# Optimization experiments

Hardware: AMD Instinct MI355X
Metric: run time of the kernel (lower is better)

## Reference

```python
import jax, jax.numpy as jnp
import numpy as np

D = 256        # d_model
NH = 8         # nhead
L = 2          # num_layers
FF = 1024      # dim_feedforward
HD = D // NH   # head dim
LN_EPS = 1e-5
M_EPS = 1e-9


def setup_inputs() -> dict:
    key = jax.random.key(0)
    ks = jax.random.split(key, 8)
    B, N, E = 8, 1024, 16384
    s = 0.02
    inp = {
        "H": jax.random.normal(ks[0], (B, N, D), jnp.float32),
        "edge_index": jax.random.randint(ks[1], (B, 2, E), 0, N),
        "m": jax.random.uniform(ks[2], (B, E), jnp.float32),
        # transformer encoder params, stacked over layers
        "Wqkv": jax.random.normal(ks[3], (L, 3 * D, D), jnp.float32) * s,
        "bqkv": jnp.zeros((L, 3 * D), jnp.float32),
        "Wo": jax.random.normal(ks[4], (L, D, D), jnp.float32) * s,
        "bo": jnp.zeros((L, D), jnp.float32),
        "ln1_w": jnp.ones((L, D), jnp.float32),
        "ln1_b": jnp.zeros((L, D), jnp.float32),
        "W1": jax.random.normal(ks[5], (L, FF, D), jnp.float32) * s,
        "b1": jnp.zeros((L, FF), jnp.float32),
        "W2": jax.random.normal(ks[6], (L, D, FF), jnp.float32) * s,
        "b2": jnp.zeros((L, D), jnp.float32),
        "ln2_w": jnp.ones((L, D), jnp.float32),
        "ln2_b": jnp.zeros((L, D), jnp.float32),
        "lnf_w": jnp.ones((D,), jnp.float32),
        "lnf_b": jnp.zeros((D,), jnp.float32),
    }
    return inp


def layer_norm(x, w, b):
    mu = jnp.mean(x, axis=-1, keepdims=True)
    var = jnp.mean(jnp.square(x - mu), axis=-1, keepdims=True)
    return (x - mu) * jax.lax.rsqrt(var + LN_EPS) * w + b


def build_bias(edge_index, m, N):
    # per-graph: -inf everywhere, 0 on diag, log(m+eps) symmetrically on edges
    bias = jnp.full((N, N), -jnp.inf, jnp.float32)
    d = jnp.arange(N)
    bias = bias.at[d, d].set(0.0)
    bv = jnp.log(m + M_EPS)
    row, col = edge_index[0], edge_index[1]
    bias = bias.at[row, col].set(bv)
    bias = bias.at[col, row].set(bv)
    return bias


def mha(x, bias, Wqkv, bqkv, Wo, bo):
    B, N, d = x.shape
    qkv = x @ Wqkv.T + bqkv                          # [B,N,3D]
    q, k, v = jnp.split(qkv, 3, axis=-1)
    def heads(t):
        return t.reshape(B, N, NH, HD).transpose(0, 2, 1, 3)  # [B,NH,N,HD]
    q, k, v = heads(q), heads(k), heads(v)
    scores = jnp.einsum("bhnd,bhmd->bhnm", q, k) / np.sqrt(HD)
    scores = scores + bias[:, None]                  # same bias for all heads
    attn = jax.nn.softmax(scores, axis=-1)
    out = jnp.einsum("bhnm,bhmd->bhnd", attn, v)
    out = out.transpose(0, 2, 1, 3).reshape(B, N, d)
    return out @ Wo.T + bo


def reference(H, edge_index, m, Wqkv, bqkv, Wo, bo, ln1_w, ln1_b, W1, b1,
              W2, b2, ln2_w, ln2_b, lnf_w, lnf_b):
    B, N, _ = H.shape
    bias = jax.vmap(lambda ei, mm: build_bias(ei, mm, N))(edge_index, m)  # [B,N,N]
    x = H
    for l in range(L):  # small fixed layer count
        a = mha(x, bias, Wqkv[l], bqkv[l], Wo[l], bo[l])
        x = layer_norm(x + a, ln1_w[l], ln1_b[l])
        f = jax.nn.gelu(x @ W1[l].T + b1[l], approximate=False) @ W2[l].T + b2[l]
        x = layer_norm(x + f, ln2_w[l], ln2_b[l])
    return layer_norm(x, lnf_w, lnf_b)
```

## Files before the change

kernel.cpp:

```cpp
#include <hip/hip_runtime.h>
#include <hip/hip_bf16.h>
#include <math.h>

typedef __bf16 bf16_t;
typedef __attribute__((ext_vector_type(8))) __bf16 bf16x8;
typedef __attribute__((ext_vector_type(4))) __bf16 bf16x4;
typedef __attribute__((ext_vector_type(4))) float f32x4;

#define BATCH 8
#define NTOK 1024
#define NEDGE 16384
#define CAP 96

__device__ __forceinline__ void gload_lds16(const void* g, void* l) {
  __builtin_amdgcn_global_load_lds(
      (const __attribute__((address_space(1))) unsigned int*)(uintptr_t)g,
      (__attribute__((address_space(3))) unsigned int*)(unsigned int)(uintptr_t)l,
      16, 0, 0);
}

__global__ void k_pre(int4* __restrict__ cnt,
                      const float* __restrict__ H, const float* __restrict__ Wqkv,
                      const float* __restrict__ Wo, const float* __restrict__ W1,
                      const float* __restrict__ W2, bf16_t* __restrict__ xb,
                      bf16_t* __restrict__ wqkvb, bf16_t* __restrict__ wob,
                      bf16_t* __restrict__ w1b, bf16_t* __restrict__ w2b) {
  int i = blockIdx.x * 256 + threadIdx.x;
  if (blockIdx.x < 8) {
    int4 z = {0, 0, 0, 0};
    cnt[i] = z;
  }
  const float* s; bf16_t* d; int off;
  if (i < 524288)      { s = H;    d = xb;    off = i; }
  else if (i < 622592) { s = Wqkv; d = wqkvb; off = i - 524288; }
  else if (i < 655360) { s = Wo;   d = wob;   off = i - 622592; }
  else if (i < 786432) { s = W1;   d = w1b;   off = i - 655360; }
  else if (i < 917504) { s = W2;   d = w2b;   off = i - 786432; }
  else return;
  float4 v = ((const float4*)s)[off];
  bf16x4 o;
  o[0] = (bf16_t)v.x; o[1] = (bf16_t)v.y; o[2] = (bf16_t)v.z; o[3] = (bf16_t)v.w;
  ((bf16x4*)d)[off] = o;
}

__global__ void k_scatter2(const int* __restrict__ ei, int* __restrict__ cnt,
                           int* __restrict__ ent) {
  int idx = blockIdx.x * 256 + threadIdx.x;
  if (idx >= BATCH * NEDGE) return;
  int b = idx >> 14;
  int e = idx & (NEDGE - 1);
  const int* eb = ei + (size_t)b * 2 * NEDGE;
  int r = eb[e], c = eb[NEDGE + e];
  int rowr = (b << 10) + r, rowc = (b << 10) + c;
  int q = atomicAdd(cnt + rowr, 1);
  if (q < CAP) ent[rowr * CAP + q] = ((e + 1) << 10) | c;
  q = atomicAdd(cnt + rowc, 1);
  if (q < CAP) ent[rowc * CAP + q] = ((NEDGE + e + 1) << 10) | r;
}

__global__ __launch_bounds__(256) void k_build2(
    const int* __restrict__ cnt, const int* __restrict__ ent,
    const float* __restrict__ mptr,
    int* __restrict__ nbcol, float* __restrict__ nbval, int* __restrict__ nbcnt) {
  const int w = threadIdx.x >> 6;
  const int l = threadIdx.x & 63;
  const int row = blockIdx.x * 4 + w;
  const int i = row & 1023;
  const int b = row >> 10;
  __shared__ int sE[4][CAP];
  __shared__ int sW[4][CAP];
  const int n = min(cnt[row], CAP);
  for (int j = l; j < n; j += 64) sE[w][j] = ent[(size_t)row * CAP + j];
  __syncthreads();

  bool dcov_l = false;
  bool win[2] = {false, false};
  int myc[2], myp[2];
#pragma unroll
  for (int s = 0; s < 2; ++s) {
    int k = s * 64 + l;
    if (k < n) {
      int pk = sE[w][k], ck = pk & 1023;
      myc[s] = ck; myp[s] = pk;
      bool wn = true;
      for (int j = 0; j < n; ++j) {
        int pj = sE[w][j];
        if ((pj & 1023) == ck && pj > pk) wn = false;
      }
      win[s] = wn;
      sW[w][k] = wn ? 1 : 0;
      if (ck == i) dcov_l = true;
    }
  }
  const bool dcov = __any(dcov_l);
  unsigned long long m0 = __ballot(win[0]);
  unsigned long long m1 = __ballot(win[1]);
  if (l == 0) nbcnt[row] = __popcll(m0) + __popcll(m1) + (dcov ? 0 : 1);

#pragma unroll
  for (int s = 0; s < 2; ++s) {
    int k = s * 64 + l;
    if (k < n && win[s]) {
      int pos = 0;
      for (int j = 0; j < n; ++j)
        if (sW[w][j] && (sE[w][j] & 1023) < myc[s]) ++pos;
      if (!dcov && i < myc[s]) ++pos;
      int e = ((myp[s] >> 10) - 1) & (NEDGE - 1);
      float v = logf(mptr[(size_t)b * NEDGE + e] + 1e-9f);
      if (pos < CAP) {
        nbcol[(size_t)row * CAP + pos] = myc[s];
        nbval[(size_t)row * CAP + pos] = v;
      }
    }
  }
  if (!dcov && l == 0) {
    int pos = 0;
    for (int j = 0; j < n; ++j)
      if (sW[w][j] && (sE[w][j] & 1023) < i) ++pos;
    nbcol[(size_t)row * CAP + pos] = i;
    nbval[(size_t)row * CAP + pos] = 0.f;
  }
}

template <int EPI, int BM>
__global__ __launch_bounds__(256) void gemm_bt(
    const bf16_t* __restrict__ A, const bf16_t* __restrict__ Bw,
    const float* __restrict__ bias, bf16_t* __restrict__ Cb,
    int M, int N, int K) {
  constexpr int MI = BM / 32;
  __shared__ bf16_t As[2][BM * 64];
  __shared__ bf16_t Bs[2][128 * 64];
  const int t = threadIdx.x;
  const int l = t & 63;
  const int w = t >> 6;
  const int wr = w >> 1, wc = w & 1;
  const int bm = blockIdx.y * BM, bn = blockIdx.x * 128;

  f32x4 acc[MI][4] = {};

  auto stage = [&](int buf, int k0) {
#pragma unroll
    for (int i = 0; i < BM / 32; ++i) {
      int idx = i * 2048 + t * 8;
      int row = idx >> 6, col = idx & 63;
      gload_lds16(A + (size_t)(bm + row) * K + (k0 + col), (void*)(&As[buf][0] + i * 2048 + w * 512));
    }
#pragma unroll
    for (int i = 0; i < 4; ++i) {
      int idx = i * 2048 + t * 8;
      int row = idx >> 6, col = idx & 63;
      gload_lds16(Bw + (size_t)(bn + row) * K + (k0 + col), (void*)(&Bs[buf][0] + i * 2048 + w * 512));
    }
  };

  const int nt = K >> 6;
  stage(0, 0);
  asm volatile("s_waitcnt vmcnt(0)" ::: "memory");
  __syncthreads();
  for (int kt = 0; kt < nt; ++kt) {
    const int cur = kt & 1;
    if (kt + 1 < nt) stage(cur ^ 1, (kt + 1) << 6);
#pragma unroll
    for (int kk = 0; kk < 2; ++kk) {
      bf16x8 af[MI], bfr[4];
#pragma unroll
      for (int mi = 0; mi < MI; ++mi)
        af[mi] = *(const bf16x8*)(&As[cur][0] + (wr * (BM / 2) + mi * 16 + (l & 15)) * 64 + kk * 32 + (l >> 4) * 8);
#pragma unroll
      for (int ni = 0; ni < 4; ++ni)
        bfr[ni] = *(const bf16x8*)(&Bs[cur][0] + (wc * 64 + ni * 16 + (l & 15)) * 64 + kk * 32 + (l >> 4) * 8);
#pragma unroll
      for (int mi = 0; mi < MI; ++mi)
#pragma unroll
        for (int ni = 0; ni < 4; ++ni)
          acc[mi][ni] = __builtin_amdgcn_mfma_f32_16x16x32_bf16(af[mi], bfr[ni], acc[mi][ni], 0, 0, 0);
    }
    asm volatile("s_waitcnt vmcnt(0)" ::: "memory");
    __syncthreads();
  }

  const int r0 = (l >> 4) * 4;
  const int cc = l & 15;
#pragma unroll
  for (int mi = 0; mi < MI; ++mi) {
#pragma unroll
    for (int ni = 0; ni < 4; ++ni) {
      int col = bn + wc * 64 + ni * 16 + cc;
      float bv = bias[col];
#pragma unroll
      for (int r = 0; r < 4; ++r) {
        int row = bm + wr * (BM / 2) + mi * 16 + r0 + r;
        float v = acc[mi][ni][r] + bv;
        if (EPI == 1)
          v = 0.5f * v * (1.f + erff(v * 0.70710678118654752f));
        Cb[(size_t)row * N + col] = (bf16_t)v;
      }
    }
  }
}

__global__ __launch_bounds__(256) void k_attn_oproj(
    const bf16_t* __restrict__ qkvb,
    const int* __restrict__ nbcol, const float* __restrict__ nbval,
    const int* __restrict__ nbcnt,
    const bf16_t* __restrict__ Wo, const float* __restrict__ bo,
    const bf16_t* __restrict__ residb,
    const float* __restrict__ lnw, const float* __restrict__ lnb,
    bf16_t* __restrict__ xbout) {
  __shared__ __align__(16) char smem[57856];
  bf16_t* Bs    = (bf16_t*)smem;
  bf16_t* ao    = (bf16_t*)(smem + 32768);
  float*  s_s   = (float*)(smem + 41216);
  int*    s_col = (int*)(smem + 53632);
  float*  s_bia = (float*)(smem + 55168);
  float*  E     = (float*)(smem + 41216);
  const int t = threadIdx.x, l = t & 63, w = t >> 6;
  const int b = blockIdx.x & 7;
  const int bm = (b << 10) + (blockIdx.x >> 3) * 16;

  auto stageB = [&](int k0) {
#pragma unroll
    for (int i = 0; i < 8; ++i) {
      int rr = (w * 8 + i) * 8 + (l >> 3), col = (l & 7) * 8;
      gload_lds16(Wo + (size_t)rr * 256 + (k0 + col), (void*)(Bs + (w * 8 + i) * 512));
    }
  };
  stageB(0);

  const float scale = 0.17677669529663687f;
  const int h1 = l & 7;
  for (int rr = 0; rr < 4; ++rr) {
    const int row = bm + w * 4 + rr;
    const int deg = nbcnt[row];
    asm volatile("s_waitcnt lgkmcnt(0)" ::: "memory");
    for (int j = l; j < deg; j += 64) {
      s_col[w * 96 + j] = nbcol[(size_t)row * CAP + j];
      s_bia[w * 96 + j] = nbval[(size_t)row * CAP + j];
    }
    float q[32];
    {
      const bf16x8* qp = (const bf16x8*)(qkvb + (size_t)row * 768 + h1 * 32);
#pragma unroll
      for (int u = 0; u < 4; ++u) {
        bf16x8 t8 = qp[u];
#pragma unroll
        for (int j = 0; j < 8; ++j) q[u * 8 + j] = (float)t8[j];
      }
    }
    asm volatile("s_waitcnt lgkmcnt(0)" ::: "memory");

    const int nit = (deg + 7) >> 3;
    float mx = -INFINITY;
    for (int it = 0; it < nit; ++it) {
      int idx = it * 8 + (l >> 3);
      float sc = -INFINITY;
      if (idx < deg) {
        int col = s_col[w * 96 + idx];
        const bf16x8* kr = (const bf16x8*)(qkvb + ((size_t)((b << 10) + col)) * 768 + 256 + h1 * 32);
        float d = 0.f;
#pragma unroll
        for (int u = 0; u < 4; ++u) {
          bf16x8 kv = kr[u];
#pragma unroll
          for (int j = 0; j < 8; ++j) d += (float)kv[j] * q[u * 8 + j];
        }
        sc = d * scale + s_bia[w * 96 + idx];
        s_s[(w * 8 + h1) * 97 + idx] = sc;
      }
      mx = fmaxf(mx, sc);
    }
#pragma unroll
    for (int o = 8; o < 64; o <<= 1) mx = fmaxf(mx, __shfl_xor(mx, o));
    asm volatile("s_waitcnt lgkmcnt(0)" ::: "memory");
    float lsum = 0.f;
    for (int it = 0; it < nit; ++it) {
      int idx = it * 8 + (l >> 3);
      if (idx < deg) {
        float p = __expf(s_s[(w * 8 + h1) * 97 + idx] - mx);
        s_s[(w * 8 + h1) * 97 + idx] = p;
        lsum += p;
      }
    }
#pragma unroll
    for (int o = 8; o < 64; o <<= 1) lsum += __shfl_xor(lsum, o);
    const int h3 = l >> 3;
    float den = __shfl(lsum, h3);
    asm volatile("s_waitcnt lgkmcnt(0)" ::: "memory");
    float a0 = 0.f, a1 = 0.f, a2 = 0.f, a3 = 0.f;
    const bf16_t* vbase = qkvb + ((size_t)(b << 10)) * 768 + 512 + l * 4;
#pragma unroll 4
    for (int idx = 0; idx < deg; ++idx) {
      float p = s_s[(w * 8 + h3) * 97 + idx];
      bf16x4 vv = *(const bf16x4*)(vbase + (size_t)s_col[w * 96 + idx] * 768);
      a0 += p * (float)vv[0]; a1 += p * (float)vv[1];
      a2 += p * (float)vv[2]; a3 += p * (float)vv[3];
    }
    float rden = 1.f / den;
    bf16x4 o4;
    o4[0] = (bf16_t)(a0 * rden); o4[1] = (bf16_t)(a1 * rden);
    o4[2] = (bf16_t)(a2 * rden); o4[3] = (bf16_t)(a3 * rden);
    *(bf16x4*)(ao + (w * 4 + rr) * 264 + l * 4) = o4;
  }
  asm volatile("s_waitcnt vmcnt(0) lgkmcnt(0)" ::: "memory");
  __syncthreads();

  f32x4 acc[4] = {};
  for (int kt = 0; kt < 4; ++kt) {
#pragma unroll
    for (int kk = 0; kk < 2; ++kk) {
      bf16x8 af = *(const bf16x8*)(ao + (l & 15) * 264 + kt * 64 + kk * 32 + (l >> 4) * 8);
#pragma unroll
      for (int ni = 0; ni < 4; ++ni) {
        bf16x8 bfr = *(const bf16x8*)(Bs + (w * 64 + ni * 16 + (l & 15)) * 64 + kk * 32 + (l >> 4) * 8);
        acc[ni] = __builtin_amdgcn_mfma_f32_16x16x32_bf16(af, bfr, acc[ni], 0, 0, 0);
      }
    }
    __syncthreads();
    if (kt < 3) {
      stageB((kt + 1) * 64);
      asm volatile("s_waitcnt vmcnt(0)" ::: "memory");
      __syncthreads();
    }
  }

  const int r0 = (l >> 4) * 4;
  const int cc = l & 15;
#pragma unroll
  for (int ni = 0; ni < 4; ++ni) {
    int col = w * 64 + ni * 16 + cc;
    float bv = bo[col];
#pragma unroll
    for (int r = 0; r < 4; ++r)
      E[(r0 + r) * 258 + col] = acc[ni][r] + bv;
  }
  __syncthreads();

  const int row = t >> 4;
  const int sub = t & 15;
  const float* ep = E + row * 258 + sub * 16;
  const bf16_t* rp = residb + (size_t)(bm + row) * 256 + sub * 16;
  float v[16];
  float s = 0.f;
#pragma unroll
  for (int j = 0; j < 4; ++j) {
    float4 a4 = ((const float4*)ep)[j];
    bf16x4 r4 = ((const bf16x4*)rp)[j];
    v[j * 4 + 0] = a4.x + (float)r4[0]; v[j * 4 + 1] = a4.y + (float)r4[1];
    v[j * 4 + 2] = a4.z + (float)r4[2]; v[j * 4 + 3] = a4.w + (float)r4[3];
    s += v[j * 4 + 0] + v[j * 4 + 1] + v[j * 4 + 2] + v[j * 4 + 3];
  }
#pragma unroll
  for (int o = 1; o < 16; o <<= 1) s += __shfl_xor(s, o);
  float mu = s * (1.f / 256.f);
  float e2 = 0.f;
#pragma unroll
  for (int j = 0; j < 16; ++j) { float d = v[j] - mu; e2 += d * d; }
#pragma unroll
  for (int o = 1; o < 16; o <<= 1) e2 += __shfl_xor(e2, o);
  float rs = rsqrtf(e2 * (1.f / 256.f) + 1e-5f);
  bf16_t* xbo = xbout + (size_t)(bm + row) * 256 + sub * 16;
#pragma unroll
  for (int j = 0; j < 4; ++j) {
    float4 w4 = ((const float4*)(lnw + sub * 16))[j];
    float4 b4 = ((const float4*)(lnb + sub * 16))[j];
    bf16x4 ob;
    ob[0] = (bf16_t)((v[j * 4 + 0] - mu) * rs * w4.x + b4.x);
    ob[1] = (bf16_t)((v[j * 4 + 1] - mu) * rs * w4.y + b4.y);
    ob[2] = (bf16_t)((v[j * 4 + 2] - mu) * rs * w4.z + b4.z);
    ob[3] = (bf16_t)((v[j * 4 + 3] - mu) * rs * w4.w + b4.w);
    ((bf16x4*)xbo)[j] = ob;
  }
}

template <int FIN>
__global__ __launch_bounds__(256) void gemm_ln(
    const bf16_t* __restrict__ A, const bf16_t* __restrict__ Bw,
    const float* __restrict__ bias, const bf16_t* __restrict__ residb,
    const float* __restrict__ lnw, const float* __restrict__ lnb,
    const float* __restrict__ lnfw, const float* __restrict__ lnfb,
    bf16_t* __restrict__ xbout, float* __restrict__ outf, int K) {
  __shared__ __align__(16) char smem[69632];
  bf16_t* As = (bf16_t*)smem;
  bf16_t* Bs = (bf16_t*)(smem + 4096);
  float*  E  = (float*)smem;
  const int t = threadIdx.x;
  const int l = t & 63;
  const int w = t >> 6;
  const int bm = blockIdx.x * 16;

  f32x4 acc[4] = {};

  auto stage = [&](int buf, int k0) {
    if (w < 2) {
      int row = w * 8 + (l >> 3), col = (l & 7) * 8;
      gload_lds16(A + (size_t)(bm + row) * K + (k0 + col), (void*)(As + buf * 1024 + w * 512));
    }
#pragma unroll
    for (int i = 0; i < 8; ++i) {
      int rr = (w * 8 + i) * 8 + (l >> 3), col = (l & 7) * 8;
      gload_lds16(Bw + (size_t)rr * K + (k0 + col), (void*)(Bs + buf * 16384 + (w * 8 + i) * 512));
    }
  };

  const int nt = K >> 6;
  stage(0, 0);
  asm volatile("s_waitcnt vmcnt(0)" ::: "memory");
  __syncthreads();
  for (int kt = 0; kt < nt; ++kt) {
    const int cur = kt & 1;
    if (kt + 1 < nt) stage(cur ^ 1, (kt + 1) << 6);
#pragma unroll
    for (int kk = 0; kk < 2; ++kk) {
      bf16x8 af = *(const bf16x8*)(As + cur * 1024 + (l & 15) * 64 + kk * 32 + (l >> 4) * 8);
#pragma unroll
      for (int ni = 0; ni < 4; ++ni) {
        bf16x8 bfr = *(const bf16x8*)(Bs + cur * 16384 + (w * 64 + ni * 16 + (l & 15)) * 64 + kk * 32 + (l >> 4) * 8);
        acc[ni] = __builtin_amdgcn_mfma_f32_16x16x32_bf16(af, bfr, acc[ni], 0, 0, 0);
      }
    }
    asm volatile("s_waitcnt vmcnt(0)" ::: "memory");
    __syncthreads();
  }

  const int r0 = (l >> 4) * 4;
  const int cc = l & 15;
#pragma unroll
  for (int ni = 0; ni < 4; ++ni) {
    int col = w * 64 + ni * 16 + cc;
    float bv = bias[col];
#pragma unroll
    for (int r = 0; r < 4; ++r)
      E[(r0 + r) * 258 + col] = acc[ni][r] + bv;
  }
  __syncthreads();

  const int row = t >> 4;
  const int sub = t & 15;
  const float* ep = E + row * 258 + sub * 16;
  const bf16_t* rp = residb + (size_t)(bm + row) * 256 + sub * 16;
  float v[16];
  float s = 0.f;
#pragma unroll
  for (int j = 0; j < 4; ++j) {
    float4 a4 = ((const float4*)ep)[j];
    bf16x4 r4 = ((const bf16x4*)rp)[j];
    v[j * 4 + 0] = a4.x + (float)r4[0]; v[j * 4 + 1] = a4.y + (float)r4[1];
    v[j * 4 + 2] = a4.z + (float)r4[2]; v[j * 4 + 3] = a4.w + (float)r4[3];
    s += v[j * 4 + 0] + v[j * 4 + 1] + v[j * 4 + 2] + v[j * 4 + 3];
  }
#pragma unroll
  for (int o = 1; o < 16; o <<= 1) s += __shfl_xor(s, o);
  float mu = s * (1.f / 256.f);
  float e2 = 0.f;
#pragma unroll
  for (int j = 0; j < 16; ++j) { float d = v[j] - mu; e2 += d * d; }
#pragma unroll
  for (int o = 1; o < 16; o <<= 1) e2 += __shfl_xor(e2, o);
  float rs = rsqrtf(e2 * (1.f / 256.f) + 1e-5f);
  float y[16];
#pragma unroll
  for (int j = 0; j < 4; ++j) {
    float4 w4 = ((const float4*)(lnw + sub * 16))[j];
    float4 b4 = ((const float4*)(lnb + sub * 16))[j];
    y[j * 4 + 0] = (v[j * 4 + 0] - mu) * rs * w4.x + b4.x;
    y[j * 4 + 1] = (v[j * 4 + 1] - mu) * rs * w4.y + b4.y;
    y[j * 4 + 2] = (v[j * 4 + 2] - mu) * rs * w4.z + b4.z;
    y[j * 4 + 3] = (v[j * 4 + 3] - mu) * rs * w4.w + b4.w;
  }
  if (FIN == 0) {
    bf16_t* xbo = xbout + (size_t)(bm + row) * 256 + sub * 16;
#pragma unroll
    for (int j = 0; j < 4; ++j) {
      bf16x4 ob;
      ob[0] = (bf16_t)y[j * 4 + 0]; ob[1] = (bf16_t)y[j * 4 + 1];
      ob[2] = (bf16_t)y[j * 4 + 2]; ob[3] = (bf16_t)y[j * 4 + 3];
      ((bf16x4*)xbo)[j] = ob;
    }
  } else {
    float s2 = 0.f;
#pragma unroll
    for (int j = 0; j < 16; ++j) s2 += y[j];
#pragma unroll
    for (int o = 1; o < 16; o <<= 1) s2 += __shfl_xor(s2, o);
    float mu2 = s2 * (1.f / 256.f);
    float q2 = 0.f;
#pragma unroll
    for (int j = 0; j < 16; ++j) { float d = y[j] - mu2; q2 += d * d; }
#pragma unroll
    for (int o = 1; o < 16; o <<= 1) q2 += __shfl_xor(q2, o);
    float rs2 = rsqrtf(q2 * (1.f / 256.f) + 1e-5f);
    float* xo = outf + (size_t)(bm + row) * 256 + sub * 16;
#pragma unroll
    for (int j = 0; j < 4; ++j) {
      float4 w4 = ((const float4*)(lnfw + sub * 16))[j];
      float4 b4 = ((const float4*)(lnfb + sub * 16))[j];
      float4 o4 = {(y[j * 4 + 0] - mu2) * rs2 * w4.x + b4.x,
                   (y[j * 4 + 1] - mu2) * rs2 * w4.y + b4.y,
                   (y[j * 4 + 2] - mu2) * rs2 * w4.z + b4.z,
                   (y[j * 4 + 3] - mu2) * rs2 * w4.w + b4.w};
      ((float4*)xo)[j] = o4;
    }
  }
}

extern "C" void kernel_launch(void* const* d_in, const int* in_sizes, int n_in,
                              void* d_out, int out_size, void* d_ws, size_t ws_size,
                              hipStream_t stream) {
  const float* H    = (const float*)d_in[0];
  const int*   ei   = (const int*)d_in[1];
  const float* m    = (const float*)d_in[2];
  const float* Wqkv = (const float*)d_in[3];
  const float* bqkv = (const float*)d_in[4];
  const float* Wo   = (const float*)d_in[5];
  const float* bo   = (const float*)d_in[6];
  const float* ln1w = (const float*)d_in[7];
  const float* ln1b = (const float*)d_in[8];
  const float* W1   = (const float*)d_in[9];
  const float* b1   = (const float*)d_in[10];
  const float* W2   = (const float*)d_in[11];
  const float* b2   = (const float*)d_in[12];
  const float* ln2w = (const float*)d_in[13];
  const float* ln2b = (const float*)d_in[14];
  const float* lnfw = (const float*)d_in[15];
  const float* lnfb = (const float*)d_in[16];

  char* ws = (char*)d_ws;
  size_t off = 0;
  auto alloc = [&](size_t bytes) {
    void* p = ws + off;
    off += (bytes + 255) & ~(size_t)255;
    return p;
  };

  int*    cnt   = (int*)alloc((size_t)BATCH * NTOK * 4);
  int*    ent   = (int*)alloc((size_t)BATCH * NTOK * CAP * 4);
  int*    nbcol = (int*)alloc((size_t)BATCH * NTOK * CAP * 4);
  float*  nbval = (float*)alloc((size_t)BATCH * NTOK * CAP * 4);
  int*    nbcnt = (int*)alloc((size_t)BATCH * NTOK * 4);
  bf16_t* qkvb  = (bf16_t*)alloc((size_t)8192 * 768 * 2);
  bf16_t* wqkvb = (bf16_t*)alloc((size_t)2 * 768 * 256 * 2);
  bf16_t* wob   = (bf16_t*)alloc((size_t)2 * 256 * 256 * 2);
  bf16_t* w1b   = (bf16_t*)alloc((size_t)2 * 1024 * 256 * 2);
  bf16_t* w2b   = (bf16_t*)alloc((size_t)2 * 256 * 1024 * 2);
  bf16_t* xb    = (bf16_t*)alloc((size_t)8192 * 256 * 2);
  bf16_t* x1b   = (bf16_t*)alloc((size_t)8192 * 256 * 2);
  bf16_t* ffb   = (bf16_t*)alloc((size_t)8192 * 1024 * 2);

  k_pre<<<3584, 256, 0, stream>>>((int4*)cnt, H, Wqkv, Wo, W1, W2,
                                  xb, wqkvb, wob, w1b, w2b);
  k_scatter2<<<(BATCH * NEDGE + 255) / 256, 256, 0, stream>>>(ei, cnt, ent);
  k_build2<<<BATCH * NTOK / 4, 256, 0, stream>>>(cnt, ent, m, nbcol, nbval, nbcnt);

  for (int lyr = 0; lyr < 2; ++lyr) {
    gemm_bt<3, 64><<<dim3(768 / 128, 8192 / 64), 256, 0, stream>>>(
        xb, wqkvb + (size_t)lyr * 768 * 256, bqkv + lyr * 768, qkvb, 8192, 768, 256);
    k_attn_oproj<<<512, 256, 0, stream>>>(
        qkvb, nbcol, nbval, nbcnt,
        wob + (size_t)lyr * 256 * 256, bo + lyr * 256, xb,
        ln1w + lyr * 256, ln1b + lyr * 256, x1b);
    gemm_bt<1, 128><<<dim3(1024 / 128, 8192 / 128), 256, 0, stream>>>(
        x1b, w1b + (size_t)lyr * 1024 * 256, b1 + lyr * 1024, ffb, 8192, 1024, 256);
    if (lyr == 0) {
      gemm_ln<0><<<512, 256, 0, stream>>>(
          ffb, w2b + (size_t)lyr * 256 * 1024, b2 + lyr * 256, x1b,
          ln2w + lyr * 256, ln2b + lyr * 256, nullptr, nullptr, xb, nullptr, 1024);
    } else {
      gemm_ln<1><<<512, 256, 0, stream>>>(
          ffb, w2b + (size_t)lyr * 256 * 1024, b2 + lyr * 256, x1b,
          ln2w + lyr * 256, ln2b + lyr * 256, lnfw, lnfb, nullptr, (float*)d_out, 1024);
    }
  }
}
```

Before: 195.1 us.

## Stream W2 fragments into registers and preload full A tile in gemm_ln

The FFN down-projection+LayerNorm kernel no longer stages B (weight) tiles through shared memory with per-iteration barriers. Each wave now loads its weight fragments straight from global memory into a triple-buffered register ring. The full 16x1024 A row-block is loaded into padded LDS once up front. This removes most barriers and cuts LDS footprint, which should raise occupancy. The cost is higher register pressure and uncoalesced-ish direct global loads of weights, which are re-read by all 512 blocks and depend on L2 hits.

After: 232.0 us. +18.9%, slower.

```diff
diff --git a/kernel.cpp b/kernel.cpp
--- a/kernel.cpp
+++ b/kernel.cpp
@@ -378,49 +378,52 @@
     const float* __restrict__ bias, const bf16_t* __restrict__ residb,
     const float* __restrict__ lnw, const float* __restrict__ lnb,
     const float* __restrict__ lnfw, const float* __restrict__ lnfb,
-    bf16_t* __restrict__ xbout, float* __restrict__ outf, int K) {
-  __shared__ __align__(16) char smem[69632];
+    bf16_t* __restrict__ xbout, float* __restrict__ outf) {
+  constexpr int K = 1024, NT = 16;
+  __shared__ __align__(16) char smem[33024];
   bf16_t* As = (bf16_t*)smem;
-  bf16_t* Bs = (bf16_t*)(smem + 4096);
   float*  E  = (float*)smem;
   const int t = threadIdx.x;
   const int l = t & 63;
   const int w = t >> 6;
   const int bm = blockIdx.x * 16;
 
+#pragma unroll
+  for (int c = 0; c < 8; ++c) {
+    int f = t + c * 256;
+    int row = f >> 7, c16 = f & 127;
+    bf16x8 v = *(const bf16x8*)(A + (size_t)(bm + row) * K + c16 * 8);
+    *(bf16x8*)(As + row * 1032 + c16 * 8) = v;
+  }
+  __syncthreads();
+
   f32x4 acc[4] = {};
-
-  auto stage = [&](int buf, int k0) {
-    if (w < 2) {
-      int row = w * 8 + (l >> 3), col = (l & 7) * 8;
-      gload_lds16(A + (size_t)(bm + row) * K + (k0 + col), (void*)(As + buf * 1024 + w * 512));
-    }
-#pragma unroll
-    for (int i = 0; i < 8; ++i) {
-      int rr = (w * 8 + i) * 8 + (l >> 3), col = (l & 7) * 8;
-      gload_lds16(Bw + (size_t)rr * K + (k0 + col), (void*)(Bs + buf * 16384 + (w * 8 + i) * 512));
-    }
-  };
-
-  const int nt = K >> 6;
-  stage(0, 0);
-  asm volatile("s_waitcnt vmcnt(0)" ::: "memory");
-  __syncthreads();
-  for (int kt = 0; kt < nt; ++kt) {
-    const int cur = kt & 1;
-    if (kt + 1 < nt) stage(cur ^ 1, (kt + 1) << 6);
+  bf16x8 breg[3][8];
+  const bf16_t* bbase = Bw + (size_t)(w * 64 + (l & 15)) * K + (l >> 4) * 8;
+#define LOADB(slot, kt)                                                        \
+  {                                                                            \
+    _Pragma("unroll")                                                          \
+    for (int ni = 0; ni < 4; ++ni)                                             \
+      _Pragma("unroll")                                                        \
+      for (int kk = 0; kk < 2; ++kk)                                           \
+        breg[slot][ni * 2 + kk] =                                              \
+            *(const bf16x8*)(bbase + (size_t)(ni * 16) * K + (kt) * 64 + kk * 32); \
+  }
+  LOADB(0, 0)
+  LOADB(1, 1)
+#pragma unroll
+  for (int kt = 0; kt < NT; ++kt) {
+    if (kt + 2 < NT) LOADB((kt + 2) % 3, kt + 2)
 #pragma unroll
     for (int kk = 0; kk < 2; ++kk) {
-      bf16x8 af = *(const bf16x8*)(As + cur * 1024 + (l & 15) * 64 + kk * 32 + (l >> 4) * 8);
-#pragma unroll
-      for (int ni = 0; ni < 4; ++ni) {
-        bf16x8 bfr = *(const bf16x8*)(Bs + cur * 16384 + (w * 64 + ni * 16 + (l & 15)) * 64 + kk * 32 + (l >> 4) * 8);
-        acc[ni] = __builtin_amdgcn_mfma_f32_16x16x32_bf16(af, bfr, acc[ni], 0, 0, 0);
-      }
-    }
-    asm volatile("s_waitcnt vmcnt(0)" ::: "memory");
-    __syncthreads();
-  }
+      bf16x8 af = *(const bf16x8*)(As + (l & 15) * 1032 + kt * 64 + kk * 32 + (l >> 4) * 8);
+#pragma unroll
+      for (int ni = 0; ni < 4; ++ni)
+        acc[ni] = __builtin_amdgcn_mfma_f32_16x16x32_bf16(af, breg[kt % 3][ni * 2 + kk], acc[ni], 0, 0, 0);
+    }
+  }
+#undef LOADB
+  __syncthreads();
 
   const int r0 = (l >> 4) * 4;
   const int cc = l & 15;
@@ -563,11 +566,11 @@
     if (lyr == 0) {
       gemm_ln<0><<<512, 256, 0, stream>>>(
           ffb, w2b + (size_t)lyr * 256 * 1024, b2 + lyr * 256, x1b,
-          ln2w + lyr * 256, ln2b + lyr * 256, nullptr, nullptr, xb, nullptr, 1024);
+          ln2w + lyr * 256, ln2b + lyr * 256, nullptr, nullptr, xb, nullptr);
     } else {
       gemm_ln<1><<<512, 256, 0, stream>>>(
           ffb, w2b + (size_t)lyr * 256 * 1024, b2 + lyr * 256, x1b,
-          ln2w + lyr * 256, ln2b + lyr * 256, lnfw, lnfb, nullptr, (float*)d_out, 1024);
-    }
-  }
-}
+          ln2w + lyr * 256, ln2b + lyr * 256, lnfw, lnfb, nullptr, (float*)d_out);
+    }
+  }
+}
```
